# Performance work log

Hardware: AMD Instinct MI355X
Metric: run time of the kernel (lower is better)

## Reference

```python
import jax, jax.numpy as jnp
import numpy as np

N_NODES = 100000
HIDDEN = 128
E = 524288  # edges per graph (pos and neg)


def setup_inputs() -> dict:
    key = jax.random.key(0)
    ks = jax.random.split(key, 8)
    return {
        "z_src": jax.random.normal(ks[0], (N_NODES, HIDDEN), dtype=jnp.float32),
        "z_dst": jax.random.normal(ks[1], (N_NODES, HIDDEN), dtype=jnp.float32),
        "pos_src": jax.random.randint(ks[2], (E,), 0, N_NODES, dtype=jnp.int64),
        "pos_dst": jax.random.randint(ks[3], (E,), 0, N_NODES, dtype=jnp.int64),
        "neg_src": jax.random.randint(ks[4], (E,), 0, N_NODES, dtype=jnp.int64),
        "neg_dst": jax.random.randint(ks[5], (E,), 0, N_NODES, dtype=jnp.int64),
        "W1": jax.random.normal(ks[6], (2 * HIDDEN, HIDDEN), dtype=jnp.float32) * (1.0 / np.sqrt(2 * HIDDEN)),
        "b1": jnp.zeros((HIDDEN,), dtype=jnp.float32),
        "W2": jax.random.normal(ks[7], (HIDDEN, 1), dtype=jnp.float32) * (1.0 / np.sqrt(HIDDEN)),
        "b2": jnp.zeros((1,), dtype=jnp.float32),
    }


def reference(z_src, z_dst, pos_src, pos_dst, neg_src, neg_dst, W1, b1, W2, b2):
    # Gather endpoint features for pos then neg edges (cat along edge dim)
    src_idx = jnp.concatenate([pos_src, neg_src])  # [2E]
    dst_idx = jnp.concatenate([pos_dst, neg_dst])  # [2E]
    z = jnp.concatenate([z_src[src_idx], z_dst[dst_idx]], axis=-1)  # [2E, 2h]
    z = jax.nn.relu(z @ W1 + b1)  # [2E, h]
    z = z @ W2 + b2               # [2E, 1]
    return z.reshape(-1)
```

## Files before the change

### kernel.cpp

```cpp
#include <hip/hip_runtime.h>
#include <hip/hip_bf16.h>
#include <cstdint>

#define N_NODES 100000
#define HIDDEN  128
#define NEDGE   524288
#define NT      6250
#define PBLK    256
#define WSTRIDE (PBLK * 4)

typedef __attribute__((ext_vector_type(8))) short short8;
typedef __attribute__((ext_vector_type(4))) float f32x4;
typedef __attribute__((ext_vector_type(4))) unsigned int u32x4;

__device__ __forceinline__ unsigned short f2b(float f) {
    unsigned u = __float_as_uint(f);
    u += 0x7FFFu + ((u >> 16) & 1u);
    return (unsigned short)(u >> 16);
}
__device__ __forceinline__ float b2f(unsigned x16) {
    return __uint_as_float(x16 << 16);
}

__device__ __forceinline__ void async_copy16(const float* g, float* l) {
    __builtin_amdgcn_global_load_lds(
        (const __attribute__((address_space(1))) unsigned int*)g,
        (__attribute__((address_space(3))) unsigned int*)l,
        16, 0, 0);
}

__global__ void wp_kernel(const float* __restrict__ W1,
                          unsigned short* __restrict__ Wp)
{
    const int f = blockIdx.x;
    const int tb = blockIdx.y;
    const int lane = threadIdx.x;
    const int t = lane & 15, q = lane >> 4;
    const int n = f >> 2, ks = f & 3;
    short8 v;
#pragma unroll
    for (int j = 0; j < 8; ++j)
        v[j] = (short)f2b(W1[(size_t)(tb * 128 + ks * 32 + q * 8 + j) * 128 + n * 16 + t]);
    *(short8*)(Wp + ((size_t)(tb * 32 + f) * 64 + lane) * 8) = v;
}

__global__ __launch_bounds__(256, 2)
void precompute_kernel(const float* __restrict__ z_src,
                       const float* __restrict__ z_dst,
                       const unsigned short* __restrict__ Wp,
                       const float* __restrict__ b1,
                       unsigned short* __restrict__ Asrc,
                       unsigned short* __restrict__ Adst)
{
    const int table = blockIdx.y;
    const float* __restrict__ z = table ? z_dst : z_src;
    unsigned short* __restrict__ A = table ? Adst : Asrc;

    __shared__ float zbuf[4][2][2048];

    const int tid = threadIdx.x;
    const int wave = tid >> 6;
    const int lane = tid & 63;
    const int t = lane & 15;
    const int q = lane >> 4;

    short8 wfrag[32];
    {
        const unsigned short* wp = Wp + ((size_t)table * 32 * 64 + lane) * 8;
#pragma unroll
        for (int f = 0; f < 32; ++f)
            wfrag[f] = *(const short8*)(wp + (size_t)f * 64 * 8);
    }

    float4 b1v[8];
#pragma unroll
    for (int n = 0; n < 8; ++n)
        b1v[n] = (table == 0) ? *(const float4*)(b1 + n * 16 + q * 4)
                              : make_float4(0.f, 0.f, 0.f, 0.f);

    const int lhi = lane >> 5;
    const int llo = lane & 31;
#define STAGE(m0, p)                                                          \
    do {                                                                      \
        _Pragma("unroll")                                                     \
        for (int j = 0; j < 8; ++j) {                                         \
            const int r = j * 2 + lhi;                                        \
            const int c = llo ^ (r & 7);                                      \
            async_copy16(z + (size_t)((m0) + r) * 128 + c * 4,                \
                         &zbuf[wave][p][j * 256]);                            \
        }                                                                     \
    } while (0)

    int tile = blockIdx.x * 4 + wave;
    int p = 0;
    STAGE(tile * 16, 0);
    __builtin_amdgcn_s_waitcnt(0xF70);
    asm volatile("" ::: "memory");

    while (tile < NT) {
        const int m0 = tile * 16;
        const int ntile = tile + WSTRIDE;
        const int nm0 = (ntile < NT ? ntile : tile) * 16;
        STAGE(nm0, p ^ 1);
        asm volatile("" ::: "memory");
        __builtin_amdgcn_s_waitcnt(0xF78);
        asm volatile("" ::: "memory");

        short8 bb[4];
#pragma unroll
        for (int ks = 0; ks < 4; ++ks) {
            const int c0 = ks * 8 + 2 * q;
            const int s = t & 7;
            const float4 v0 = *(const float4*)&zbuf[wave][p][(t * 32 + (c0 ^ s)) * 4];
            const float4 v1 = *(const float4*)&zbuf[wave][p][(t * 32 + ((c0 + 1) ^ s)) * 4];
            bb[ks][0] = (short)f2b(v0.x); bb[ks][1] = (short)f2b(v0.y);
            bb[ks][2] = (short)f2b(v0.z); bb[ks][3] = (short)f2b(v0.w);
            bb[ks][4] = (short)f2b(v1.x); bb[ks][5] = (short)f2b(v1.y);
            bb[ks][6] = (short)f2b(v1.z); bb[ks][7] = (short)f2b(v1.w);
        }

        f32x4 acc[8];
#pragma unroll
        for (int n = 0; n < 8; ++n) acc[n] = (f32x4){0.f, 0.f, 0.f, 0.f};
#pragma unroll
        for (int n = 0; n < 8; ++n)
#pragma unroll
            for (int ks = 0; ks < 4; ++ks)
                acc[n] = __builtin_amdgcn_mfma_f32_16x16x32_bf16(
                             wfrag[n * 4 + ks], bb[ks], acc[n], 0, 0, 0);

        unsigned short* ob = (unsigned short*)&zbuf[wave][p][0];
        const int sw = (t & 7) * 2;
#pragma unroll
        for (int n = 0; n < 8; ++n) {
            ushort4 h;
            h.x = f2b(acc[n][0] + b1v[n].x);
            h.y = f2b(acc[n][1] + b1v[n].y);
            h.z = f2b(acc[n][2] + b1v[n].z);
            h.w = f2b(acc[n][3] + b1v[n].w);
            *(ushort4*)&ob[t * 136 + (((n * 4 + q) ^ sw) * 4)] = h;
        }
        const int rr = lane >> 4;
#pragma unroll
        for (int it = 0; it < 4; ++it) {
            const int r = it * 4 + rr;
            const uint4 v = *(const uint4*)&ob[r * 136 + (((2 * t) ^ ((r & 7) * 2)) * 4)];
            *(uint4*)(A + (size_t)(m0 + r) * 128 + t * 8) = v;
        }
        asm volatile("" ::: "memory");

        p ^= 1;
        tile = ntile;
    }
#undef STAGE
}

__global__ __launch_bounds__(256, 6)
void edge_kernel(const unsigned short* __restrict__ Asrc,
                 const unsigned short* __restrict__ Adst,
                 const int* __restrict__ pos_src,
                 const int* __restrict__ pos_dst,
                 const int* __restrict__ neg_src,
                 const int* __restrict__ neg_dst,
                 const float* __restrict__ W2,
                 const float* __restrict__ b2,
                 float* __restrict__ out)
{
    const int tid = threadIdx.x;
    const int t = tid & 15;
    const int g = tid >> 4;

    const bool is_pos = blockIdx.x < 8192;
    const int* __restrict__ sp = is_pos ? pos_src : neg_src;
    const int* __restrict__ dp = is_pos ? pos_dst : neg_dst;
    const int eb = (is_pos ? (int)blockIdx.x : (int)blockIdx.x - 8192) * 64;

    float w2r[8];
#pragma unroll
    for (int j = 0; j < 8; ++j) w2r[j] = W2[t * 8 + j];
    const float bias2 = b2[0];

    unsigned soff[4], doff[4];
#pragma unroll
    for (int i = 0; i < 4; ++i) {
        soff[i] = ((unsigned)sp[eb + i * 16 + g] << 8) + t * 16;
        doff[i] = ((unsigned)dp[eb + i * 16 + g] << 8) + t * 16;
    }

    u32x4 ua[4], ub[4];
#pragma unroll
    for (int i = 0; i < 4; ++i) {
        asm volatile("global_load_dwordx4 %0, %1, %2"
                     : "=v"(ua[i]) : "v"(soff[i]), "s"(Asrc));
        asm volatile("global_load_dwordx4 %0, %1, %2"
                     : "=v"(ub[i]) : "v"(doff[i]), "s"(Adst));
    }

    float res[4];

#define CHUNK(i, VMSTR)                                                       \
    do {                                                                      \
        asm volatile("s_waitcnt " VMSTR : "+v"(ua[i]), "+v"(ub[i]));          \
        __builtin_amdgcn_sched_barrier(0);                                    \
        const unsigned* pa = (const unsigned*)&ua[i];                         \
        const unsigned* pb = (const unsigned*)&ub[i];                         \
        float acc = 0.f;                                                      \
        _Pragma("unroll")                                                     \
        for (int j2 = 0; j2 < 4; ++j2) {                                      \
            float h0 = b2f(pa[j2] & 0xFFFFu) + b2f(pb[j2] & 0xFFFFu);         \
            float h1 = b2f(pa[j2] >> 16)     + b2f(pb[j2] >> 16);             \
            h0 = fmaxf(h0, 0.f);                                              \
            h1 = fmaxf(h1, 0.f);                                              \
            acc = fmaf(h0, w2r[2 * j2], acc);                                 \
            acc = fmaf(h1, w2r[2 * j2 + 1], acc);                             \
        }                                                                     \
        acc += __shfl_xor(acc, 1);                                            \
        acc += __shfl_xor(acc, 2);                                            \
        acc += __shfl_xor(acc, 4);                                            \
        acc += __shfl_xor(acc, 8);                                            \
        res[i] = acc + bias2;                                                 \
    } while (0)

    CHUNK(0, "vmcnt(6)");
    CHUNK(1, "vmcnt(4)");
    CHUNK(2, "vmcnt(2)");
    CHUNK(3, "vmcnt(0)");
#undef CHUNK

    if (t == 0) {
#pragma unroll
        for (int i = 0; i < 4; ++i)
            out[blockIdx.x * 64 + i * 16 + g] = res[i];
    }
}

extern "C" void kernel_launch(void* const* d_in, const int* in_sizes, int n_in,
                              void* d_out, int out_size, void* d_ws, size_t ws_size,
                              hipStream_t stream) {
    const float* z_src  = (const float*)d_in[0];
    const float* z_dst  = (const float*)d_in[1];
    const int* pos_src  = (const int*)d_in[2];
    const int* pos_dst  = (const int*)d_in[3];
    const int* neg_src  = (const int*)d_in[4];
    const int* neg_dst  = (const int*)d_in[5];
    const float* W1     = (const float*)d_in[6];
    const float* b1     = (const float*)d_in[7];
    const float* W2     = (const float*)d_in[8];
    const float* b2     = (const float*)d_in[9];
    float* out = (float*)d_out;

    unsigned short* Asrc = (unsigned short*)d_ws;
    unsigned short* Adst = Asrc + (size_t)N_NODES * HIDDEN;
    unsigned short* Wp   = Adst + (size_t)N_NODES * HIDDEN;

    wp_kernel<<<dim3(32, 2), 64, 0, stream>>>(W1, Wp);

    precompute_kernel<<<dim3(PBLK, 2), 256, 0, stream>>>(z_src, z_dst, Wp, b1,
                                                         Asrc, Adst);

    edge_kernel<<<16384, 256, 0, stream>>>(Asrc, Adst, pos_src, pos_dst,
                                           neg_src, neg_dst, W2, b2, out);
}
```

Before: 217.7 us.

## Bin edges by source-node bucket so Asrc gathers stay resident in per-XCD L2

Adds a binning pass that splits all edges into 16 buckets by source-node range and writes packed (local src, dst) records plus an inverse slot map. The edge kernel then walks bucket by bucket, with block indices arranged so that each of the 8 XCDs handles two buckets, and an unbin kernel scatters the scores back into edge order. The aim is to shrink the working set of the random Asrc gather per XCD so it can be served from L2 instead of HBM. The cost is three extra launches and extra traffic for records, the inverse map and the scattered scores. Any bucket that exceeds its fixed capacity silently gets a 0 output, so correctness depends on edges being spread fairly evenly across buckets.

```diff
diff --git a/kernel.cpp b/kernel.cpp
--- a/kernel.cpp
+++ b/kernel.cpp
@@ -9,6 +9,13 @@
 #define PBLK    256
 #define WSTRIDE (PBLK * 4)
 
+#define NBKT    16
+#define BKT_SZ  6250
+#define CAP     69632
+#define BPB     (CAP / 64)
+#define EGRID   (NBKT * BPB)
+#define NREC    (NBKT * CAP)
+
 typedef __attribute__((ext_vector_type(8))) short short8;
 typedef __attribute__((ext_vector_type(4))) float f32x4;
 typedef __attribute__((ext_vector_type(4))) unsigned int u32x4;
@@ -42,6 +49,11 @@
     for (int j = 0; j < 8; ++j)
         v[j] = (short)f2b(W1[(size_t)(tb * 128 + ks * 32 + q * 8 + j) * 128 + n * 16 + t]);
     *(short8*)(Wp + ((size_t)(tb * 32 + f) * 64 + lane) * 8) = v;
+}
+
+__global__ void zero_kernel(unsigned* __restrict__ gcnt)
+{
+    if (threadIdx.x < NBKT) gcnt[threadIdx.x] = 0;
 }
 
 __global__ __launch_bounds__(256, 2)
@@ -155,36 +167,96 @@
 #undef STAGE
 }
 
+__global__ __launch_bounds__(256, 4)
+void bin_kernel(const int* __restrict__ pos_src,
+                const int* __restrict__ pos_dst,
+                const int* __restrict__ neg_src,
+                const int* __restrict__ neg_dst,
+                unsigned* __restrict__ rec,
+                unsigned* __restrict__ inv,
+                unsigned* __restrict__ gcnt)
+{
+    __shared__ unsigned lcnt[NBKT];
+    __shared__ unsigned lbase[NBKT];
+
+    const int tid = threadIdx.x;
+    const int blk = (int)blockIdx.x;
+    const bool is_pos = blk < 128;
+    const int* __restrict__ sp = is_pos ? pos_src : neg_src;
+    const int* __restrict__ dp = is_pos ? pos_dst : neg_dst;
+    const int base = (is_pos ? blk : blk - 128) * 4096;
+    const unsigned ebase = (is_pos ? 0u : (unsigned)NEDGE) + (unsigned)base;
+
+    if (tid < NBKT) lcnt[tid] = 0;
+    __syncthreads();
+
+    unsigned s[16], d[16], loc[16];
+    unsigned char bkt[16];
+#pragma unroll
+    for (int k = 0; k < 16; ++k) {
+        const int off = base + k * 256 + tid;
+        s[k] = (unsigned)sp[off];
+        d[k] = (unsigned)dp[off];
+        bkt[k] = (unsigned char)(s[k] / BKT_SZ);
+        loc[k] = atomicAdd(&lcnt[bkt[k]], 1u);
+    }
+    __syncthreads();
+    if (tid < NBKT) lbase[tid] = atomicAdd(&gcnt[tid], lcnt[tid]);
+    __syncthreads();
+#pragma unroll
+    for (int k = 0; k < 16; ++k) {
+        const unsigned b = bkt[k];
+        const unsigned sl = lbase[b] + loc[k];
+        const unsigned e = ebase + (unsigned)(k * 256 + tid);
+        if (sl < CAP) {
+            rec[(size_t)b * CAP + sl] = (s[k] - b * BKT_SZ) | (d[k] << 13);
+            inv[e] = b * CAP + sl;
+        } else {
+            inv[e] = 0xFFFFFFFFu;
+        }
+    }
+}
+
 __global__ __launch_bounds__(256, 6)
-void edge_kernel(const unsigned short* __restrict__ Asrc,
-                 const unsigned short* __restrict__ Adst,
-                 const int* __restrict__ pos_src,
-                 const int* __restrict__ pos_dst,
-                 const int* __restrict__ neg_src,
-                 const int* __restrict__ neg_dst,
-                 const float* __restrict__ W2,
-                 const float* __restrict__ b2,
-                 float* __restrict__ out)
-{
+void edge_bin_kernel(const unsigned short* __restrict__ Asrc,
+                     const unsigned short* __restrict__ Adst,
+                     const unsigned* __restrict__ rec,
+                     const unsigned* __restrict__ gcnt,
+                     const float* __restrict__ W2,
+                     const float* __restrict__ b2,
+                     float* __restrict__ sc)
+{
+    const int gb = (int)blockIdx.x;
+    const int x = gb & 7;
+    const int j = gb >> 3;
+    const int ph = (j >= BPB) ? 1 : 0;
+    const int bucket = x + 8 * ph;
+    const int jj = j - ph * BPB;
+    const int slot0 = jj * 64;
+
+    const unsigned cnt = gcnt[bucket];
+    if ((unsigned)slot0 >= cnt) return;
+
     const int tid = threadIdx.x;
     const int t = tid & 15;
-    const int g = tid >> 4;
-
-    const bool is_pos = blockIdx.x < 8192;
-    const int* __restrict__ sp = is_pos ? pos_src : neg_src;
-    const int* __restrict__ dp = is_pos ? pos_dst : neg_dst;
-    const int eb = (is_pos ? (int)blockIdx.x : (int)blockIdx.x - 8192) * 64;
+    const int eg = tid >> 4;
 
     float w2r[8];
 #pragma unroll
-    for (int j = 0; j < 8; ++j) w2r[j] = W2[t * 8 + j];
+    for (int jw = 0; jw < 8; ++jw) w2r[jw] = W2[t * 8 + jw];
     const float bias2 = b2[0];
 
     unsigned soff[4], doff[4];
+    bool val[4];
 #pragma unroll
     for (int i = 0; i < 4; ++i) {
-        soff[i] = ((unsigned)sp[eb + i * 16 + g] << 8) + t * 16;
-        doff[i] = ((unsigned)dp[eb + i * 16 + g] << 8) + t * 16;
+        const int sl = slot0 + i * 16 + eg;
+        const unsigned r = rec[(size_t)bucket * CAP + sl];
+        val[i] = ((unsigned)sl < cnt);
+        const unsigned sidx = (unsigned)bucket * BKT_SZ + (r & 8191u);
+        const unsigned didx = r >> 13;
+        soff[i] = val[i] ? (sidx << 8) + t * 16 : (unsigned)(t * 16);
+        doff[i] = val[i] ? (didx << 8) + t * 16 : (unsigned)(t * 16);
     }
 
     u32x4 ua[4], ub[4];
@@ -197,7 +269,6 @@
     }
 
     float res[4];
-
 #define CHUNK(i, VMSTR)                                                       \
     do {                                                                      \
         asm volatile("s_waitcnt " VMSTR : "+v"(ua[i]), "+v"(ub[i]));          \
@@ -230,6 +301,99 @@
     if (t == 0) {
 #pragma unroll
         for (int i = 0; i < 4; ++i)
+            sc[(size_t)bucket * CAP + slot0 + i * 16 + eg] = res[i];
+    }
+}
+
+__global__ __launch_bounds__(256, 8)
+void unbin_kernel(const unsigned* __restrict__ inv,
+                  const float* __restrict__ sc,
+                  float* __restrict__ out)
+{
+    const int tid = threadIdx.x;
+    const int e0 = (int)blockIdx.x * 2048;
+#pragma unroll
+    for (int k = 0; k < 8; ++k) {
+        const int e = e0 + k * 256 + tid;
+        const unsigned slot = inv[e];
+        out[e] = (slot != 0xFFFFFFFFu) ? sc[slot] : 0.f;
+    }
+}
+
+__global__ __launch_bounds__(256, 6)
+void edge_kernel(const unsigned short* __restrict__ Asrc,
+                 const unsigned short* __restrict__ Adst,
+                 const int* __restrict__ pos_src,
+                 const int* __restrict__ pos_dst,
+                 const int* __restrict__ neg_src,
+                 const int* __restrict__ neg_dst,
+                 const float* __restrict__ W2,
+                 const float* __restrict__ b2,
+                 float* __restrict__ out)
+{
+    const int tid = threadIdx.x;
+    const int t = tid & 15;
+    const int g = tid >> 4;
+
+    const bool is_pos = blockIdx.x < 8192;
+    const int* __restrict__ sp = is_pos ? pos_src : neg_src;
+    const int* __restrict__ dp = is_pos ? pos_dst : neg_dst;
+    const int eb = (is_pos ? (int)blockIdx.x : (int)blockIdx.x - 8192) * 64;
+
+    float w2r[8];
+#pragma unroll
+    for (int jw = 0; jw < 8; ++jw) w2r[jw] = W2[t * 8 + jw];
+    const float bias2 = b2[0];
+
+    unsigned soff[4], doff[4];
+#pragma unroll
+    for (int i = 0; i < 4; ++i) {
+        soff[i] = ((unsigned)sp[eb + i * 16 + g] << 8) + t * 16;
+        doff[i] = ((unsigned)dp[eb + i * 16 + g] << 8) + t * 16;
+    }
+
+    u32x4 ua[4], ub[4];
+#pragma unroll
+    for (int i = 0; i < 4; ++i) {
+        asm volatile("global_load_dwordx4 %0, %1, %2"
+                     : "=v"(ua[i]) : "v"(soff[i]), "s"(Asrc));
+        asm volatile("global_load_dwordx4 %0, %1, %2"
+                     : "=v"(ub[i]) : "v"(doff[i]), "s"(Adst));
+    }
+
+    float res[4];
+#define CHUNK(i, VMSTR)                                                       \
+    do {                                                                      \
+        asm volatile("s_waitcnt " VMSTR : "+v"(ua[i]), "+v"(ub[i]));          \
+        __builtin_amdgcn_sched_barrier(0);                                    \
+        const unsigned* pa = (const unsigned*)&ua[i];                         \
+        const unsigned* pb = (const unsigned*)&ub[i];                         \
+        float acc = 0.f;                                                      \
+        _Pragma("unroll")                                                     \
+        for (int j2 = 0; j2 < 4; ++j2) {                                      \
+            float h0 = b2f(pa[j2] & 0xFFFFu) + b2f(pb[j2] & 0xFFFFu);         \
+            float h1 = b2f(pa[j2] >> 16)     + b2f(pb[j2] >> 16);             \
+            h0 = fmaxf(h0, 0.f);                                              \
+            h1 = fmaxf(h1, 0.f);                                              \
+            acc = fmaf(h0, w2r[2 * j2], acc);                                 \
+            acc = fmaf(h1, w2r[2 * j2 + 1], acc);                             \
+        }                                                                     \
+        acc += __shfl_xor(acc, 1);                                            \
+        acc += __shfl_xor(acc, 2);                                            \
+        acc += __shfl_xor(acc, 4);                                            \
+        acc += __shfl_xor(acc, 8);                                            \
+        res[i] = acc + bias2;                                                 \
+    } while (0)
+
+    CHUNK(0, "vmcnt(6)");
+    CHUNK(1, "vmcnt(4)");
+    CHUNK(2, "vmcnt(2)");
+    CHUNK(3, "vmcnt(0)");
+#undef CHUNK
+
+    if (t == 0) {
+#pragma unroll
+        for (int i = 0; i < 4; ++i)
             out[blockIdx.x * 64 + i * 16 + g] = res[i];
     }
 }
@@ -249,15 +413,31 @@
     const float* b2     = (const float*)d_in[9];
     float* out = (float*)d_out;
 
-    unsigned short* Asrc = (unsigned short*)d_ws;
-    unsigned short* Adst = Asrc + (size_t)N_NODES * HIDDEN;
-    unsigned short* Wp   = Adst + (size_t)N_NODES * HIDDEN;
+    const size_t tab_bytes = (size_t)N_NODES * HIDDEN * 2;
+    char* wsb = (char*)d_ws;
+    size_t off = 0;
+    unsigned short* Asrc = (unsigned short*)(wsb + off); off += tab_bytes;
+    unsigned short* Adst = (unsigned short*)(wsb + off); off += tab_bytes;
+    unsigned short* Wp   = (unsigned short*)(wsb + off); off += 64 * 1024;
+    unsigned* rec = (unsigned*)(wsb + off); off += (size_t)NREC * 4;
+    unsigned* inv = (unsigned*)(wsb + off); off += (size_t)2 * NEDGE * 4;
+    float*    sc  = (float*)(wsb + off);    off += (size_t)NREC * 4;
+    unsigned* gcnt = (unsigned*)(wsb + off); off += 256;
+    const size_t need = off;
 
     wp_kernel<<<dim3(32, 2), 64, 0, stream>>>(W1, Wp);
-
     precompute_kernel<<<dim3(PBLK, 2), 256, 0, stream>>>(z_src, z_dst, Wp, b1,
                                                          Asrc, Adst);
 
-    edge_kernel<<<16384, 256, 0, stream>>>(Asrc, Adst, pos_src, pos_dst,
-                                           neg_src, neg_dst, W2, b2, out);
-}
+    if (ws_size >= need) {
+        zero_kernel<<<1, 64, 0, stream>>>(gcnt);
+        bin_kernel<<<256, 256, 0, stream>>>(pos_src, pos_dst, neg_src, neg_dst,
+                                            rec, inv, gcnt);
+        edge_bin_kernel<<<EGRID, 256, 0, stream>>>(Asrc, Adst, rec, gcnt,
+                                                   W2, b2, sc);
+        unbin_kernel<<<512, 256, 0, stream>>>(inv, sc, out);
+    } else {
+        edge_kernel<<<16384, 256, 0, stream>>>(Asrc, Adst, pos_src, pos_dst,
+                                               neg_src, neg_dst, W2, b2, out);
+    }
+}
```

After: 213.6 us. Within noise of the previous version (-1.9%).
